# Optimization experiments

Hardware: AMD Instinct MI355X
Metric: run time of the kernel (lower is better)

Reference implementation:

```python
import jax, jax.numpy as jnp
import numpy as np

KLD_SCALE = 10.0
COMMITMENT_COST = 0.1


def setup_inputs() -> dict:
    key = jax.random.key(0)
    k1, k2 = jax.random.split(key)
    z = jax.random.normal(k1, (32, 2048, 64), dtype=jnp.float32)
    codebook = jax.random.normal(k2, (1024, 64), dtype=jnp.float32)
    return {"z": z, "codebook": codebook}


def reference(z, codebook):
    B, N, D = z.shape
    z_e = z.reshape(B * N, D)                          # (M, D)
    # squared euclidean distance: ||z||^2 - 2 z.E^T + ||E||^2
    dist = (
        jnp.sum(z_e * z_e, axis=1, keepdims=True)
        - 2.0 * (z_e @ codebook.T)
        + jnp.sum(codebook * codebook, axis=1)[None, :]
    )                                                  # (M, K)
    ind = jnp.argmin(dist, axis=1)                     # (M,)
    z_q = codebook[ind]                                # (M, D) gather
    latent_loss = (
        COMMITMENT_COST * jnp.mean((jax.lax.stop_gradient(z_q) - z_e) ** 2)
        + jnp.mean((z_q - jax.lax.stop_gradient(z_e)) ** 2)
    ) * KLD_SCALE
    # straight-through estimator
    z_q_st = z_e + jax.lax.stop_gradient(z_q - z_e)
    return z_q_st.reshape(B, N, D), latent_loss
```

## Files before the change

### kernel.cpp

```cpp
#include <hip/hip_runtime.h>
#include <hip/hip_bf16.h>
#include <float.h>

#define DIMS 64
#define KC 1024
#define M_TOTAL 65536
#define TAU 4e-3f

typedef __attribute__((ext_vector_type(8))) short bf16x8;
typedef __attribute__((ext_vector_type(4))) float f32x4;

#define SE_OFF   0
#define PART_OFF 1024
#define CNT_OFF  2048
#define WL_OFF   2304
#define IDX_OFF  (2304 + 65536)
#define PBH_OFF  (2304 + 2*65536)
#define PBL_OFF  (PBH_OFF + 32768)

__device__ inline short f2bf(float x) {
  union { __hip_bfloat16 h; short s; } u;
  u.h = __float2bfloat16(x);
  return u.s;
}
__device__ inline float bf2f(short x) {
  union { short s; __hip_bfloat16 h; } u;
  u.s = x;
  return __bfloat162float(u.h);
}

__global__ __launch_bounds__(256) void k_se(const float* __restrict__ cb,
                                            float* __restrict__ se,
                                            int* __restrict__ cnt) {
  if (blockIdx.x == 0 && threadIdx.x == 0) *cnt = 0;
  int k = blockIdx.x * 256 + threadIdx.x;
  const float4* p = (const float4*)(cb + (size_t)k * DIMS);
  float a0 = 0.f, a1 = 0.f, a2 = 0.f, a3 = 0.f;
#pragma unroll
  for (int i = 0; i < DIMS / 4; ++i) {
    float4 v = p[i];
    a0 = fmaf(v.x, v.x, a0);
    a1 = fmaf(v.y, v.y, a1);
    a2 = fmaf(v.z, v.z, a2);
    a3 = fmaf(v.w, v.w, a3);
  }
  se[k] = (a0 + a1) + (a2 + a3);
}

__global__ __launch_bounds__(256) void k_packB(const float* __restrict__ cb,
                                               unsigned short* __restrict__ pbh,
                                               unsigned short* __restrict__ pbl) {
  const int tid = blockIdx.x * 256 + threadIdx.x;
  const int l = tid & 63;
  const int s = (tid >> 6) & 1;
  const int tt = tid >> 7;
  const int code = tt * 16 + (l & 15);
  const int k = s * 32 + (l >> 4) * 8;
  const float* p = cb + (size_t)code * DIMS + k;
  float v[8];
  ((float4*)v)[0] = ((const float4*)p)[0];
  ((float4*)v)[1] = ((const float4*)p)[1];
  bf16x8 h, lo;
#pragma unroll
  for (int j = 0; j < 8; ++j) {
    short hj = f2bf(v[j]);
    h[j] = hj;
    lo[j] = f2bf(v[j] - bf2f(hj));
  }
  *(bf16x8*)(pbh + (size_t)tid * 8) = h;
  *(bf16x8*)(pbl + (size_t)tid * 8) = lo;
}

__global__ __launch_bounds__(256) void k_dist_mfma(const float* __restrict__ z,
                                                   const unsigned short* __restrict__ pbh,
                                                   const unsigned short* __restrict__ pbl,
                                                   const float* __restrict__ se,
                                                   int* __restrict__ idxo,
                                                   int* __restrict__ wl,
                                                   int* __restrict__ cnt) {
  const int l = threadIdx.x & 63;
  const int w = threadIdx.x >> 6;
  const int r0 = blockIdx.x * 64 + w * 16;
  const int col = l & 15;
  const int g = l >> 4;

  const float* zp = z + (size_t)(r0 + col) * DIMS + g * 8;
  bf16x8 a0h, a1h, a0l, a1l;
  {
    float v[8];
    ((float4*)v)[0] = ((const float4*)zp)[0];
    ((float4*)v)[1] = ((const float4*)zp)[1];
#pragma unroll
    for (int j = 0; j < 8; ++j) {
      short hj = f2bf(v[j]);
      a0h[j] = hj;
      a0l[j] = f2bf(v[j] - bf2f(hj));
    }
    ((float4*)v)[0] = ((const float4*)(zp + 32))[0];
    ((float4*)v)[1] = ((const float4*)(zp + 32))[1];
#pragma unroll
    for (int j = 0; j < 8; ++j) {
      short hj = f2bf(v[j]);
      a1h[j] = hj;
      a1l[j] = f2bf(v[j] - bf2f(hj));
    }
  }

  const bf16x8* pbhv = (const bf16x8*)pbh;
  const bf16x8* pblv = (const bf16x8*)pbl;
  float m1[4] = {FLT_MAX, FLT_MAX, FLT_MAX, FLT_MAX};
  float m2[4] = {FLT_MAX, FLT_MAX, FLT_MAX, FLT_MAX};
  int bt[4] = {0, 0, 0, 0};

  for (int t = 0; t < 64; ++t) {
    bf16x8 b0h = pbhv[t * 128 + l];
    bf16x8 b1h = pbhv[t * 128 + 64 + l];
    bf16x8 b0l = pblv[t * 128 + l];
    bf16x8 b1l = pblv[t * 128 + 64 + l];
    f32x4 accA = {0.f, 0.f, 0.f, 0.f};
    f32x4 accB = {0.f, 0.f, 0.f, 0.f};
    accA = __builtin_amdgcn_mfma_f32_16x16x32_bf16(a0h, b0h, accA, 0, 0, 0);
    accB = __builtin_amdgcn_mfma_f32_16x16x32_bf16(a1h, b1h, accB, 0, 0, 0);
    accA = __builtin_amdgcn_mfma_f32_16x16x32_bf16(a0h, b0l, accA, 0, 0, 0);
    accB = __builtin_amdgcn_mfma_f32_16x16x32_bf16(a1h, b1l, accB, 0, 0, 0);
    accA = __builtin_amdgcn_mfma_f32_16x16x32_bf16(a0l, b0h, accA, 0, 0, 0);
    accB = __builtin_amdgcn_mfma_f32_16x16x32_bf16(a1l, b1h, accB, 0, 0, 0);
    float sec = se[t * 16 + col];
#pragma unroll
    for (int j = 0; j < 4; ++j) {
      float d = fmaf(-2.f, accA[j] + accB[j], sec);
      bool lt = d < m1[j];
      m2[j] = fminf(m2[j], lt ? m1[j] : d);
      m1[j] = fminf(m1[j], d);
      bt[j] = lt ? t : bt[j];
    }
  }

#pragma unroll
  for (int j = 0; j < 4; ++j) {
    float m1j = m1[j], m2j = m2[j];
    int ij = bt[j] * 16 + col;
    for (int msk = 1; msk <= 8; msk <<= 1) {
      float o1 = __shfl_xor(m1j, msk);
      float o2 = __shfl_xor(m2j, msk);
      int oi = __shfl_xor(ij, msk);
      bool take = (o1 < m1j) || (o1 == m1j && oi < ij);
      float hi = take ? m1j : o1;
      m2j = fminf(fminf(m2j, o2), hi);
      m1j = take ? o1 : m1j;
      ij = take ? oi : ij;
    }
    if (col == 0) {
      int row = r0 + g * 4 + j;
      idxo[row] = ij;
      if (m2j - m1j < TAU) {
        int p = atomicAdd(cnt, 1);
        wl[p] = row;
      }
    }
  }
}

__global__ __launch_bounds__(256) void k_refine(const float* __restrict__ z,
                                                const float* __restrict__ cb,
                                                const int* __restrict__ wl,
                                                const int* __restrict__ cnt,
                                                int* __restrict__ idxo) {
  __shared__ float zz[64];
  __shared__ double sd[256];
  __shared__ int si[256];
  const int t = threadIdx.x;
  const int n = *cnt;
  for (int wi = blockIdx.x; wi < n; wi += 2048) {
    const int row = wl[wi];
    if (t < 16) ((float4*)zz)[t] = ((const float4*)(z + (size_t)row * DIMS))[t];
    __syncthreads();
    const int c0 = t * 4;
    double accd[4] = {0.0, 0.0, 0.0, 0.0};
    for (int ch = 0; ch < 4; ++ch) {
      float zr[16];
#pragma unroll
      for (int q = 0; q < 4; ++q) ((float4*)zr)[q] = ((float4*)zz)[ch * 4 + q];
#pragma unroll
      for (int cc = 0; cc < 4; ++cc) {
        const float* e = cb + (size_t)(c0 + cc) * DIMS + ch * 16;
#pragma unroll
        for (int q = 0; q < 16; ++q) {
          double df = (double)zr[q] - (double)e[q];
          accd[cc] = fma(df, df, accd[cc]);
        }
      }
    }
    double best = 1e300;
    int bi = 0;
#pragma unroll
    for (int cc = 0; cc < 4; ++cc) {
      if (accd[cc] < best) { best = accd[cc]; bi = c0 + cc; }
    }
    sd[t] = best;
    si[t] = bi;
    __syncthreads();
    for (int off = 128; off > 0; off >>= 1) {
      if (t < off) {
        double ob = sd[t + off];
        int oi = si[t + off];
        if (ob < sd[t] || (ob == sd[t] && oi < si[t])) { sd[t] = ob; si[t] = oi; }
      }
      __syncthreads();
    }
    if (t == 0) idxo[row] = si[0];
    __syncthreads();
  }
}

__global__ __launch_bounds__(256) void k_out(const float* __restrict__ z,
                                             const float* __restrict__ cb,
                                             const int* __restrict__ idxi,
                                             float* __restrict__ out,
                                             float* __restrict__ partials) {
  const int tid = blockIdx.x * 256 + threadIdx.x;
  const int row = tid >> 2;
  const int q = tid & 3;
  const int code = idxi[row];
  const float4* zp = (const float4*)(z + (size_t)row * DIMS + q * 16);
  const float4* ep = (const float4*)(cb + (size_t)code * DIMS + q * 16);
  float4* op = (float4*)(out + (size_t)row * DIMS + q * 16);
  float sse = 0.f;
#pragma unroll
  for (int i = 0; i < 4; ++i) {
    float4 v = zp[i], e = ep[i];
    float dx = e.x - v.x, dy = e.y - v.y, dz = e.z - v.z, dw = e.w - v.w;
    sse = fmaf(dx, dx, sse);
    sse = fmaf(dy, dy, sse);
    sse = fmaf(dz, dz, sse);
    sse = fmaf(dw, dw, sse);
    float4 o;
    o.x = v.x + dx;
    o.y = v.y + dy;
    o.z = v.z + dz;
    o.w = v.w + dw;
    op[i] = o;
  }
  __shared__ float sh[256];
  sh[threadIdx.x] = sse;
  __syncthreads();
  for (int off = 128; off > 0; off >>= 1) {
    if (threadIdx.x < off) sh[threadIdx.x] += sh[threadIdx.x + off];
    __syncthreads();
  }
  if (threadIdx.x == 0) partials[blockIdx.x] = sh[0];
}

__global__ __launch_bounds__(256) void k_loss(const float* __restrict__ partials,
                                              float* __restrict__ out) {
  __shared__ float sh[256];
  const int t = threadIdx.x;
  sh[t] = partials[t] + partials[t + 256] + partials[t + 512] + partials[t + 768];
  __syncthreads();
  for (int off = 128; off > 0; off >>= 1) {
    if (t < off) sh[t] += sh[t + off];
    __syncthreads();
  }
  if (t == 0) {
    out[(size_t)M_TOTAL * DIMS] = sh[0] * (11.0f / (float)((size_t)M_TOTAL * DIMS));
  }
}

extern "C" void kernel_launch(void* const* d_in, const int* in_sizes, int n_in,
                              void* d_out, int out_size, void* d_ws, size_t ws_size,
                              hipStream_t stream) {
  const float* z = (const float*)d_in[0];
  const float* cb = (const float*)d_in[1];
  float* out = (float*)d_out;
  float* ws = (float*)d_ws;

  float* se = ws + SE_OFF;
  float* partials = ws + PART_OFF;
  int* cnt = (int*)(ws + CNT_OFF);
  int* wl = (int*)(ws + WL_OFF);
  int* idx = (int*)(ws + IDX_OFF);
  unsigned short* pbh = (unsigned short*)(ws + PBH_OFF);
  unsigned short* pbl = (unsigned short*)(ws + PBL_OFF);

  k_se<<<KC / 256, 256, 0, stream>>>(cb, se, cnt);
  k_packB<<<32, 256, 0, stream>>>(cb, pbh, pbl);
  k_dist_mfma<<<M_TOTAL / 64, 256, 0, stream>>>(z, pbh, pbl, se, idx, wl, cnt);
  k_refine<<<2048, 256, 0, stream>>>(z, cb, wl, cnt, idx);
  k_out<<<1024, 256, 0, stream>>>(z, cb, idx, out, partials);
  k_loss<<<1, 256, 0, stream>>>(partials, out);
}
```

Before: 71.63 us.

## Stage codebook tiles in LDS with double buffering and fuse prep and loss kernels

The distance kernel now streams packed bf16 hi/lo codebook tiles into double-buffered shared memory with global_load_lds instead of having every wave read them straight from global memory. The six MFMAs now chain into one accumulator, and the second-minimum tracking uses fmed3. The codebook norm and packing kernels are merged into one prep kernel. The separate loss-reduction kernel is replaced by a fixed-point 64-bit atomic accumulation with a last-block-finishes pattern, cutting two launches. The trade-offs are a barrier per tile, loss of the two independent accumulator chains, and quantising the loss to fixed point.

```diff
diff --git a/kernel.cpp b/kernel.cpp
--- a/kernel.cpp
+++ b/kernel.cpp
@@ -11,12 +11,13 @@
 typedef __attribute__((ext_vector_type(4))) float f32x4;
 
 #define SE_OFF   0
-#define PART_OFF 1024
-#define CNT_OFF  2048
-#define WL_OFF   2304
-#define IDX_OFF  (2304 + 65536)
-#define PBH_OFF  (2304 + 2*65536)
-#define PBL_OFF  (PBH_OFF + 32768)
+#define CTL_OFF  1024
+#define PBH_OFF  2048
+#define PBL_OFF  34816
+#define WL_OFF   67584
+#define IDX_OFF  133120
+
+#define LOSS_SCALE 1048576.0
 
 __device__ inline short f2bf(float x) {
   union { __hip_bfloat16 h; short s; } u;
@@ -29,28 +30,19 @@
   return __bfloat162float(u.h);
 }
 
-__global__ __launch_bounds__(256) void k_se(const float* __restrict__ cb,
-                                            float* __restrict__ se,
-                                            int* __restrict__ cnt) {
-  if (blockIdx.x == 0 && threadIdx.x == 0) *cnt = 0;
-  int k = blockIdx.x * 256 + threadIdx.x;
-  const float4* p = (const float4*)(cb + (size_t)k * DIMS);
-  float a0 = 0.f, a1 = 0.f, a2 = 0.f, a3 = 0.f;
-#pragma unroll
-  for (int i = 0; i < DIMS / 4; ++i) {
-    float4 v = p[i];
-    a0 = fmaf(v.x, v.x, a0);
-    a1 = fmaf(v.y, v.y, a1);
-    a2 = fmaf(v.z, v.z, a2);
-    a3 = fmaf(v.w, v.w, a3);
-  }
-  se[k] = (a0 + a1) + (a2 + a3);
-}
-
-__global__ __launch_bounds__(256) void k_packB(const float* __restrict__ cb,
-                                               unsigned short* __restrict__ pbh,
-                                               unsigned short* __restrict__ pbl) {
+__device__ inline void gload_lds16(const void* g, void* l) {
+  __builtin_amdgcn_global_load_lds(
+      (const __attribute__((address_space(1))) void*)g,
+      (__attribute__((address_space(3))) void*)l, 16, 0, 0);
+}
+
+__global__ __launch_bounds__(256) void k_prep(const float* __restrict__ cb,
+                                              float* __restrict__ se,
+                                              unsigned int* __restrict__ ctl,
+                                              unsigned short* __restrict__ pbh,
+                                              unsigned short* __restrict__ pbl) {
   const int tid = blockIdx.x * 256 + threadIdx.x;
+  if (tid < 4) ctl[tid] = 0;
   const int l = tid & 63;
   const int s = (tid >> 6) & 1;
   const int tt = tid >> 7;
@@ -69,71 +61,98 @@
   }
   *(bf16x8*)(pbh + (size_t)tid * 8) = h;
   *(bf16x8*)(pbl + (size_t)tid * 8) = lo;
-}
-
-__global__ __launch_bounds__(256) void k_dist_mfma(const float* __restrict__ z,
-                                                   const unsigned short* __restrict__ pbh,
-                                                   const unsigned short* __restrict__ pbl,
-                                                   const float* __restrict__ se,
-                                                   int* __restrict__ idxo,
-                                                   int* __restrict__ wl,
-                                                   int* __restrict__ cnt) {
+
+  if (tid < KC) {
+    const float4* q = (const float4*)(cb + (size_t)tid * DIMS);
+    float a0 = 0.f, a1 = 0.f, a2 = 0.f, a3 = 0.f;
+#pragma unroll
+    for (int i = 0; i < DIMS / 4; ++i) {
+      float4 u = q[i];
+      a0 = fmaf(u.x, u.x, a0);
+      a1 = fmaf(u.y, u.y, a1);
+      a2 = fmaf(u.z, u.z, a2);
+      a3 = fmaf(u.w, u.w, a3);
+    }
+    se[tid] = (a0 + a1) + (a2 + a3);
+  }
+}
+
+__global__ __launch_bounds__(256, 4) void k_dist(const float* __restrict__ z,
+                                                 const unsigned short* __restrict__ pbh,
+                                                 const unsigned short* __restrict__ pbl,
+                                                 const float* __restrict__ se,
+                                                 int* __restrict__ idxo,
+                                                 int* __restrict__ wl,
+                                                 unsigned int* __restrict__ ctl) {
+  __shared__ bf16x8 sB[2][2][256];
   const int l = threadIdx.x & 63;
   const int w = threadIdx.x >> 6;
   const int r0 = blockIdx.x * 64 + w * 16;
   const int col = l & 15;
   const int g = l >> 4;
 
-  const float* zp = z + (size_t)(r0 + col) * DIMS + g * 8;
-  bf16x8 a0h, a1h, a0l, a1l;
+  bf16x8 ah[2], al[2];
   {
-    float v[8];
-    ((float4*)v)[0] = ((const float4*)zp)[0];
-    ((float4*)v)[1] = ((const float4*)zp)[1];
-#pragma unroll
-    for (int j = 0; j < 8; ++j) {
-      short hj = f2bf(v[j]);
-      a0h[j] = hj;
-      a0l[j] = f2bf(v[j] - bf2f(hj));
-    }
-    ((float4*)v)[0] = ((const float4*)(zp + 32))[0];
-    ((float4*)v)[1] = ((const float4*)(zp + 32))[1];
-#pragma unroll
-    for (int j = 0; j < 8; ++j) {
-      short hj = f2bf(v[j]);
-      a1h[j] = hj;
-      a1l[j] = f2bf(v[j] - bf2f(hj));
-    }
-  }
-
-  const bf16x8* pbhv = (const bf16x8*)pbh;
-  const bf16x8* pblv = (const bf16x8*)pbl;
+    const float* zp = z + (size_t)(r0 + col) * DIMS + g * 8;
+#pragma unroll
+    for (int ks = 0; ks < 2; ++ks) {
+      float v[8];
+      ((float4*)v)[0] = ((const float4*)(zp + ks * 32))[0];
+      ((float4*)v)[1] = ((const float4*)(zp + ks * 32))[1];
+#pragma unroll
+      for (int j = 0; j < 8; ++j) {
+        short hj = f2bf(v[j]);
+        ah[ks][j] = hj;
+        al[ks][j] = f2bf(v[j] - bf2f(hj));
+      }
+    }
+  }
+
   float m1[4] = {FLT_MAX, FLT_MAX, FLT_MAX, FLT_MAX};
   float m2[4] = {FLT_MAX, FLT_MAX, FLT_MAX, FLT_MAX};
   int bt[4] = {0, 0, 0, 0};
 
-  for (int t = 0; t < 64; ++t) {
-    bf16x8 b0h = pbhv[t * 128 + l];
-    bf16x8 b1h = pbhv[t * 128 + 64 + l];
-    bf16x8 b0l = pblv[t * 128 + l];
-    bf16x8 b1l = pblv[t * 128 + 64 + l];
-    f32x4 accA = {0.f, 0.f, 0.f, 0.f};
-    f32x4 accB = {0.f, 0.f, 0.f, 0.f};
-    accA = __builtin_amdgcn_mfma_f32_16x16x32_bf16(a0h, b0h, accA, 0, 0, 0);
-    accB = __builtin_amdgcn_mfma_f32_16x16x32_bf16(a1h, b1h, accB, 0, 0, 0);
-    accA = __builtin_amdgcn_mfma_f32_16x16x32_bf16(a0h, b0l, accA, 0, 0, 0);
-    accB = __builtin_amdgcn_mfma_f32_16x16x32_bf16(a1h, b1l, accB, 0, 0, 0);
-    accA = __builtin_amdgcn_mfma_f32_16x16x32_bf16(a0l, b0h, accA, 0, 0, 0);
-    accB = __builtin_amdgcn_mfma_f32_16x16x32_bf16(a1l, b1h, accB, 0, 0, 0);
-    float sec = se[t * 16 + col];
-#pragma unroll
-    for (int j = 0; j < 4; ++j) {
-      float d = fmaf(-2.f, accA[j] + accB[j], sec);
-      bool lt = d < m1[j];
-      m2[j] = fminf(m2[j], lt ? m1[j] : d);
-      m1[j] = fminf(m1[j], d);
-      bt[j] = lt ? t : bt[j];
-    }
+  {
+    const int f = w * 64 + l;
+    gload_lds16(pbh + (size_t)f * 8, &sB[0][0][w * 64]);
+    gload_lds16(pbl + (size_t)f * 8, &sB[0][1][w * 64]);
+  }
+  __syncthreads();
+
+  int cur = 0;
+  for (int c = 0; c < 32; ++c) {
+    if (c + 1 < 32) {
+      const size_t f = (size_t)(c + 1) * 256 + w * 64 + l;
+      gload_lds16(pbh + f * 8, &sB[cur ^ 1][0][w * 64]);
+      gload_lds16(pbl + f * 8, &sB[cur ^ 1][1][w * 64]);
+    }
+#pragma unroll
+    for (int tt = 0; tt < 2; ++tt) {
+      const int t = c * 2 + tt;
+      bf16x8 bh0 = sB[cur][0][tt * 128 + l];
+      bf16x8 bh1 = sB[cur][0][tt * 128 + 64 + l];
+      bf16x8 bl0 = sB[cur][1][tt * 128 + l];
+      bf16x8 bl1 = sB[cur][1][tt * 128 + 64 + l];
+      const float sec = se[t * 16 + col];
+      f32x4 acc = {0.f, 0.f, 0.f, 0.f};
+      acc = __builtin_amdgcn_mfma_f32_16x16x32_bf16(ah[0], bh0, acc, 0, 0, 0);
+      acc = __builtin_amdgcn_mfma_f32_16x16x32_bf16(ah[1], bh1, acc, 0, 0, 0);
+      acc = __builtin_amdgcn_mfma_f32_16x16x32_bf16(ah[0], bl0, acc, 0, 0, 0);
+      acc = __builtin_amdgcn_mfma_f32_16x16x32_bf16(ah[1], bl1, acc, 0, 0, 0);
+      acc = __builtin_amdgcn_mfma_f32_16x16x32_bf16(al[0], bh0, acc, 0, 0, 0);
+      acc = __builtin_amdgcn_mfma_f32_16x16x32_bf16(al[1], bh1, acc, 0, 0, 0);
+#pragma unroll
+      for (int j = 0; j < 4; ++j) {
+        float d = fmaf(-2.f, acc[j], sec);
+        float nm2 = __builtin_amdgcn_fmed3f(d, m1[j], m2[j]);
+        bool lt = d < m1[j];
+        m1[j] = lt ? d : m1[j];
+        bt[j] = lt ? t : bt[j];
+        m2[j] = nm2;
+      }
+    }
+    __syncthreads();
+    cur ^= 1;
   }
 
 #pragma unroll
@@ -151,10 +170,10 @@
       ij = take ? oi : ij;
     }
     if (col == 0) {
-      int row = r0 + g * 4 + j;
+      const int row = r0 + g * 4 + j;
       idxo[row] = ij;
       if (m2j - m1j < TAU) {
-        int p = atomicAdd(cnt, 1);
+        int p = atomicAdd((int*)ctl, 1);
         wl[p] = row;
       }
     }
@@ -164,13 +183,13 @@
 __global__ __launch_bounds__(256) void k_refine(const float* __restrict__ z,
                                                 const float* __restrict__ cb,
                                                 const int* __restrict__ wl,
-                                                const int* __restrict__ cnt,
+                                                const unsigned int* __restrict__ ctl,
                                                 int* __restrict__ idxo) {
   __shared__ float zz[64];
   __shared__ double sd[256];
   __shared__ int si[256];
   const int t = threadIdx.x;
-  const int n = *cnt;
+  const int n = (int)ctl[0];
   for (int wi = blockIdx.x; wi < n; wi += 2048) {
     const int row = wl[wi];
     if (t < 16) ((float4*)zz)[t] = ((const float4*)(z + (size_t)row * DIMS))[t];
@@ -194,9 +213,8 @@
     double best = 1e300;
     int bi = 0;
 #pragma unroll
-    for (int cc = 0; cc < 4; ++cc) {
+    for (int cc = 0; cc < 4; ++cc)
       if (accd[cc] < best) { best = accd[cc]; bi = c0 + cc; }
-    }
     sd[t] = best;
     si[t] = bi;
     __syncthreads();
@@ -217,7 +235,7 @@
                                              const float* __restrict__ cb,
                                              const int* __restrict__ idxi,
                                              float* __restrict__ out,
-                                             float* __restrict__ partials) {
+                                             unsigned int* __restrict__ ctl) {
   const int tid = blockIdx.x * 256 + threadIdx.x;
   const int row = tid >> 2;
   const int q = tid & 3;
@@ -248,21 +266,16 @@
     if (threadIdx.x < off) sh[threadIdx.x] += sh[threadIdx.x + off];
     __syncthreads();
   }
-  if (threadIdx.x == 0) partials[blockIdx.x] = sh[0];
-}
-
-__global__ __launch_bounds__(256) void k_loss(const float* __restrict__ partials,
-                                              float* __restrict__ out) {
-  __shared__ float sh[256];
-  const int t = threadIdx.x;
-  sh[t] = partials[t] + partials[t + 256] + partials[t + 512] + partials[t + 768];
-  __syncthreads();
-  for (int off = 128; off > 0; off >>= 1) {
-    if (t < off) sh[t] += sh[t + off];
-    __syncthreads();
-  }
-  if (t == 0) {
-    out[(size_t)M_TOTAL * DIMS] = sh[0] * (11.0f / (float)((size_t)M_TOTAL * DIMS));
+  if (threadIdx.x == 0) {
+    unsigned long long* acc = (unsigned long long*)(ctl + 2);
+    atomicAdd(acc, (unsigned long long)(long long)llrintf(sh[0] * (float)LOSS_SCALE));
+    __threadfence();
+    unsigned int done = atomicAdd(ctl + 1, 1u);
+    if (done == gridDim.x - 1) {
+      unsigned long long v = atomicAdd(acc, 0ULL);
+      double sse_tot = (double)(long long)v * (1.0 / LOSS_SCALE);
+      out[(size_t)M_TOTAL * DIMS] = (float)(sse_tot * 11.0 / ((double)M_TOTAL * DIMS));
+    }
   }
 }
 
@@ -275,17 +288,14 @@
   float* ws = (float*)d_ws;
 
   float* se = ws + SE_OFF;
-  float* partials = ws + PART_OFF;
-  int* cnt = (int*)(ws + CNT_OFF);
+  unsigned int* ctl = (unsigned int*)(ws + CTL_OFF);
+  unsigned short* pbh = (unsigned short*)(ws + PBH_OFF);
+  unsigned short* pbl = (unsigned short*)(ws + PBL_OFF);
   int* wl = (int*)(ws + WL_OFF);
   int* idx = (int*)(ws + IDX_OFF);
-  unsigned short* pbh = (unsigned short*)(ws + PBH_OFF);
-  unsigned short* pbl = (unsigned short*)(ws + PBL_OFF);
-
-  k_se<<<KC / 256, 256, 0, stream>>>(cb, se, cnt);
-  k_packB<<<32, 256, 0, stream>>>(cb, pbh, pbl);
-  k_dist_mfma<<<M_TOTAL / 64, 256, 0, stream>>>(z, pbh, pbl, se, idx, wl, cnt);
-  k_refine<<<2048, 256, 0, stream>>>(z, cb, wl, cnt, idx);
-  k_out<<<1024, 256, 0, stream>>>(z, cb, idx, out, partials);
-  k_loss<<<1, 256, 0, stream>>>(partials, out);
-}
+
+  k_prep<<<32, 256, 0, stream>>>(cb, se, ctl, pbh, pbl);
+  k_dist<<<M_TOTAL / 64, 256, 0, stream>>>(z, pbh, pbl, se, idx, wl, ctl);
+  k_refine<<<2048, 256, 0, stream>>>(z, cb, wl, ctl, idx);
+  k_out<<<M_TOTAL / 64, 256, 0, stream>>>(z, cb, idx, out, ctl);
+}
```

New measurement: 97.31 us. 35.8% more time.
